# Kernel optimization log

Measured on AMD Instinct MI355X. Metric: run time of the kernel, lower is better.

Reference implementation:

```python
import jax, jax.numpy as jnp
import numpy as np
from jax import lax

B, N, C_IN = 8, 4096, 64
NPOINT, K = 1024, 32
MLP = [128, 128, 256]
EPS = 1e-5


def setup_inputs() -> dict:
    key = jax.random.key(0)
    ks = jax.random.split(key, 2 + len(MLP))
    inp = {
        "xyz": jax.random.normal(ks[0], (B, N, 3), jnp.float32),
        "points": jax.random.normal(ks[1], (B, N, C_IN), jnp.float32),
    }
    last = 3 + C_IN
    for i, o in enumerate(MLP):
        inp[f"W{i}"] = jax.random.normal(ks[2 + i], (o, last), jnp.float32) / np.float32(np.sqrt(last))
        inp[f"b{i}"] = jnp.zeros((o,), jnp.float32)
        inp[f"gamma{i}"] = jnp.ones((o,), jnp.float32)
        inp[f"beta{i}"] = jnp.zeros((o,), jnp.float32)
        last = o
    return inp


def farthest_point_sample(xyz, S):
    # xyz: (B,N,3) -> idx (B,S). Deterministic start at index 0 (torch uses randint).
    Bn, Nn, _ = xyz.shape
    barange = jnp.arange(Bn)

    def step(carry, _):
        distance, farthest = carry
        centroid = xyz[barange, farthest][:, None, :]            # (B,1,3)
        d = jnp.sum((xyz - centroid) ** 2, axis=-1)              # (B,N)
        distance = jnp.minimum(distance, d)
        return (distance, jnp.argmax(distance, axis=-1)), farthest

    init = (jnp.full((Bn, Nn), 1e10, xyz.dtype), jnp.zeros((Bn,), jnp.int32))
    _, cent = lax.scan(step, init, None, length=S)
    return jnp.transpose(cent)                                    # (B,S)


def _sa_forward(xyz, points, params):
    S = min(NPOINT, N)
    Kk = min(K, N)
    fps_idx = farthest_point_sample(xyz, S)                       # (B,S)
    bidx = jnp.arange(xyz.shape[0])[:, None]
    new_xyz = xyz[bidx, fps_idx]                                  # (B,S,3)
    # squared distances (B,S,N)
    dists = (jnp.sum(new_xyz ** 2, -1, keepdims=True)
             - 2.0 * jnp.einsum('bsc,bnc->bsn', new_xyz, xyz)
             + jnp.sum(xyz ** 2, -1)[:, None, :])
    _, nn_idx = lax.top_k(-dists, Kk)                             # (B,S,K)
    bidx3 = jnp.arange(xyz.shape[0])[:, None, None]
    grouped_xyz = xyz[bidx3, nn_idx]                              # (B,S,K,3)
    grouped_xyz_norm = grouped_xyz - new_xyz[:, :, None, :]
    grouped_pts = points[bidx3, nn_idx]                           # (B,S,K,C)
    feat = jnp.concatenate([grouped_xyz_norm, grouped_pts], -1)   # (B,S,K,3+C)
    for (W, b, g, be) in params:
        feat = jnp.einsum('bskc,oc->bsko', feat, W) + b           # 1x1 conv
        mean = jnp.mean(feat, axis=(0, 1, 2))
        var = jnp.var(feat, axis=(0, 1, 2))                        # biased, training-mode BN
        feat = (feat - mean) * lax.rsqrt(var + EPS) * g + be
        feat = jax.nn.relu(feat)
    out = jnp.max(feat, axis=2)                                   # max over K -> (B,S,O)
    return new_xyz, jnp.transpose(out, (0, 2, 1))                 # (B,O,S) like torch


def reference(xyz, points, W0, b0, gamma0, beta0, W1, b1, gamma1, beta1, W2, b2, gamma2, beta2):
    params = [(W0, b0, gamma0, beta0), (W1, b1, gamma1, beta1), (W2, b2, gamma2, beta2)]
    return _sa_forward(xyz, points, params)
```

## Files before the change

kernel.cpp:

```cpp
#include <hip/hip_runtime.h>
#include <cstdint>
#include <cstddef>

typedef _Float16 half8 __attribute__((ext_vector_type(8)));
typedef float f32x4 __attribute__((ext_vector_type(4)));
typedef float f32x2 __attribute__((ext_vector_type(2)));
typedef unsigned short ushort_t;

#define BB 8
#define NN 4096
#define CIN 64
#define SS 1024
#define KK 32
#define O1 128
#define O2 128
#define O3 256
#define C0 67
#define P0 104
#define P1 136
#define MTOT (BB*SS*KK)
#define NBLK 4096

__device__ __forceinline__ ushort_t f2h(float v) {
  union { _Float16 h; ushort_t u; } cv;
  cv.h = (_Float16)v;
  return cv.u;
}
__device__ __forceinline__ half8 ldv(const ushort_t* p) {
  return *(const half8*)p;
}
__device__ __forceinline__ f32x4 MF(half8 a, half8 b, f32x4 c) {
  return __builtin_amdgcn_mfma_f32_16x16x32_f16(a, b, c, 0, 0, 0);
}

template<bool MAXM>
__device__ __forceinline__ void wave_red_dpp(float& d, int& i) {
#define RED_TAKE(d2, i2) \
  { bool take = MAXM ? ((d2) > d || ((d2) == d && (i2) < i)) \
                     : ((d2) < d || ((d2) == d && (i2) < i)); \
    if (take) { d = (d2); i = (i2); } }
#define RED_DPP(CTRL) \
  { float d2_ = __int_as_float(__builtin_amdgcn_update_dpp(0, __float_as_int(d), CTRL, 0xf, 0xf, true)); \
    int   i2_ = __builtin_amdgcn_update_dpp(0, i, CTRL, 0xf, 0xf, true); \
    RED_TAKE(d2_, i2_) }
  RED_DPP(0x128)
  RED_DPP(0x124)
  RED_DPP(0x122)
  RED_DPP(0x121)
  RED_DPP(0x142)
  RED_DPP(0x143)
#undef RED_DPP
#undef RED_TAKE
}

__global__ __launch_bounds__(256, 1) void fps_kernel(const float* __restrict__ xyz,
                                                     float* __restrict__ newxyz) {
  int b = blockIdx.x, t = threadIdx.x;
  __shared__ float sxyz[NN*3];
  __shared__ float snew[SS*3];
  __shared__ __align__(16) float wpair[2][4][2];
  {
    const float4* src = (const float4*)(xyz + (size_t)b * (NN*3));
    float4* dst = (float4*)sxyz;
    for (int i = t; i < NN*3/4; i += 256) dst[i] = src[i];
  }
  __syncthreads();
  f32x2 px2[8], py2[8], pz2[8], d2[8];
#pragma unroll
  for (int j = 0; j < 8; ++j) {
    int n0 = t + 512*j, n1 = n0 + 256;
    f32x2 vx = {sxyz[n0*3+0], sxyz[n1*3+0]};
    f32x2 vy = {sxyz[n0*3+1], sxyz[n1*3+1]};
    f32x2 vz = {sxyz[n0*3+2], sxyz[n1*3+2]};
    px2[j] = vx; py2[j] = vy; pz2[j] = vz;
    f32x2 ini = {1e10f, 1e10f};
    d2[j] = ini;
  }
  float cx = sxyz[0], cy = sxyz[1], cz = sxyz[2];
  for (int s = 0; s < SS; ++s) {
    if (t == 0) {
      snew[s*3+0] = cx; snew[s*3+1] = cy; snew[s*3+2] = cz;
    }
    float bd0 = -1.f, bd1 = -1.f, bd2 = -1.f, bd3 = -1.f;
    int   bi0 = 0, bi1 = 0, bi2 = 0, bi3 = 0;
    {
#pragma clang fp contract(off)
      f32x2 c2x = {cx, cx}, c2y = {cy, cy}, c2z = {cz, cz};
#pragma unroll
      for (int j = 0; j < 8; ++j) {
        f32x2 dx = px2[j] - c2x;
        f32x2 dy = py2[j] - c2y;
        f32x2 dz = pz2[j] - c2z;
        f32x2 dd = (dx*dx + dy*dy) + dz*dz;
        float nd0 = fminf(d2[j][0], dd[0]);
        float nd1 = fminf(d2[j][1], dd[1]);
        d2[j][0] = nd0; d2[j][1] = nd1;
        int i0 = t + 512*j, i1 = i0 + 256;
        if ((j & 1) == 0) {
          if (nd0 > bd0) { bd0 = nd0; bi0 = i0; }
          if (nd1 > bd1) { bd1 = nd1; bi1 = i1; }
        } else {
          if (nd0 > bd2) { bd2 = nd0; bi2 = i0; }
          if (nd1 > bd3) { bd3 = nd1; bi3 = i1; }
        }
      }
    }
    float bd = bd0; int bi = bi0;
    if (bd1 > bd || (bd1 == bd && bi1 < bi)) { bd = bd1; bi = bi1; }
    if (bd2 > bd || (bd2 == bd && bi2 < bi)) { bd = bd2; bi = bi2; }
    if (bd3 > bd || (bd3 == bd && bi3 < bi)) { bd = bd3; bi = bi3; }

    wave_red_dpp<true>(bd, bi);

    int p = s & 1;
    if ((t & 63) == 63) {
      wpair[p][t>>6][0] = bd;
      ((int*)&wpair[p][t>>6][0])[1] = bi;
    }
    __syncthreads();
    float4 q0 = *(const float4*)&wpair[p][0][0];
    float4 q1 = *(const float4*)&wpair[p][2][0];
    float fd = q0.x; int fi = __float_as_int(q0.y);
#define CMB(dv, iv) { float od = (dv); int oi = __float_as_int(iv); \
      if (od > fd || (od == fd && oi < fi)) { fd = od; fi = oi; } }
    CMB(q0.z, q0.w) CMB(q1.x, q1.y) CMB(q1.z, q1.w)
#undef CMB
    cx = sxyz[fi*3+0]; cy = sxyz[fi*3+1]; cz = sxyz[fi*3+2];
  }
  __syncthreads();
  {
    float4* dst = (float4*)(newxyz + (size_t)b * (SS*3));
    const float4* src = (const float4*)snew;
    for (int i = t; i < SS*3/4; i += 256) dst[i] = src[i];
  }
}

__global__ __launch_bounds__(256) void knn_kernel(const float* __restrict__ xyz,
                                                  const float* __restrict__ newxyz,
                                                  int* __restrict__ nn) {
  int blk = blockIdx.x;
  int b = blk >> 10;
  int t = threadIdx.x;
  __shared__ __align__(16) float lpair[2][4][2];
  __shared__ int sidx[KK];
  float qx = newxyz[(size_t)blk*3+0];
  float qy = newxyz[(size_t)blk*3+1];
  float qz = newxyz[(size_t)blk*3+2];
  float cs = __fadd_rn(__fadd_rn(__fmul_rn(qx,qx), __fmul_rn(qy,qy)), __fmul_rn(qz,qz));
  const float* base = xyz + (size_t)b * (NN*3);
  float d[16];
#pragma unroll
  for (int j = 0; j < 16; ++j) {
    int n = t + 256*j;
    float px = base[n*3+0], py = base[n*3+1], pz = base[n*3+2];
    float xs  = __fadd_rn(__fadd_rn(__fmul_rn(px,px), __fmul_rn(py,py)), __fmul_rn(pz,pz));
    float dot = __fadd_rn(__fadd_rn(__fmul_rn(qx,px), __fmul_rn(qy,py)), __fmul_rn(qz,pz));
    d[j] = __fadd_rn(__fadd_rn(cs, -__fmul_rn(2.f, dot)), xs);
  }
  float lmin = 3.0e38f; int lidx = 0x7fffffff;
#pragma unroll
  for (int j = 0; j < 16; ++j) {
    if (d[j] < lmin) { lmin = d[j]; lidx = t + 256*j; }
  }
  for (int it = 0; it < KK; ++it) {
    float bd = lmin; int bi = lidx;
    wave_red_dpp<false>(bd, bi);
    int p = it & 1;
    if ((t & 63) == 63) {
      lpair[p][t>>6][0] = bd;
      ((int*)&lpair[p][t>>6][0])[1] = bi;
    }
    __syncthreads();
    float4 q0 = *(const float4*)&lpair[p][0][0];
    float4 q1 = *(const float4*)&lpair[p][2][0];
    float fd = q0.x; int fi = __float_as_int(q0.y);
#define CMB(dv, iv) { float od = (dv); int oi = __float_as_int(iv); \
      if (od < fd || (od == fd && oi < fi)) { fd = od; fi = oi; } }
    CMB(q0.z, q0.w) CMB(q1.x, q1.y) CMB(q1.z, q1.w)
#undef CMB
    if (t == 0) sidx[it] = fi;
    if ((fi & 255) == t) {
      int jj = fi >> 8;
#pragma unroll
      for (int j = 0; j < 16; ++j) if (j == jj) d[j] = 3.0e38f;
      lmin = 3.0e38f; lidx = 0x7fffffff;
#pragma unroll
      for (int j = 0; j < 16; ++j) {
        if (d[j] < lmin) { lmin = d[j]; lidx = t + 256*j; }
      }
    }
  }
  __syncthreads();
  if (t < KK) nn[(size_t)blk*KK + t] = sidx[t];
}

__global__ void prep_kernel(const float* __restrict__ W0, const float* __restrict__ W1,
                            const float* __restrict__ W2,
                            ushort_t* __restrict__ wb1, ushort_t* __restrict__ wb2,
                            ushort_t* __restrict__ wb3) {
  int i = blockIdx.x*256 + threadIdx.x;
  int stride = gridDim.x*256;
  const int n1 = O1*96, n2 = O2*128, n3 = O3*128;
  for (; i < n1+n2+n3; i += stride) {
    if (i < n1) {
      int o = i / 96, k = i - o*96;
      wb1[i] = (k < C0) ? f2h(W0[o*C0 + k]) : (ushort_t)0;
    } else if (i < n1+n2) {
      int j = i - n1;
      wb2[j] = f2h(W1[j]);
    } else {
      int j = i - n1 - n2;
      wb3[j] = f2h(W2[j]);
    }
  }
}

template<int NT>
__device__ __forceinline__ void stats_and_store(
    const f32x4* acc, const float* __restrict__ bias,
    float (*sred)[256][2],
    int w, int lr, int lg, int t, int blk,
    float* __restrict__ psum, float* __restrict__ psq)
{
#pragma unroll
  for (int n = 0; n < NT; ++n) {
    int c = n*16 + lr;
    float bi = bias[c];
    float x0 = acc[n][0]+bi, x1 = acc[n][1]+bi, x2 = acc[n][2]+bi, x3 = acc[n][3]+bi;
    float s4 = (x0+x1)+(x2+x3);
    float q4 = (x0*x0+x1*x1)+(x2*x2+x3*x3);
    s4 += __shfl_xor(s4, 16); s4 += __shfl_xor(s4, 32);
    q4 += __shfl_xor(q4, 16); q4 += __shfl_xor(q4, 32);
    if (lg == 0) { sred[w][c][0] = s4; sred[w][c][1] = q4; }
  }
  __syncthreads();
  if (t < NT*16) {
    float ps = (sred[0][t][0]+sred[1][t][0])+(sred[2][t][0]+sred[3][t][0]);
    float pq = (sred[0][t][1]+sred[1][t][1])+(sred[2][t][1]+sred[3][t][1]);
    psum[(size_t)t*NBLK + blk] = ps;
    psq [(size_t)t*NBLK + blk] = pq;
  }
}

__device__ __forceinline__ void stage_feat0(
    const float* __restrict__ xyz, const float* __restrict__ points,
    const float* __restrict__ newxyz, const int* __restrict__ nn,
    ushort_t* sF, int t, int b, int pr)
{
  int r = t >> 2, q = t & 3;
  int gi = r >> 5, j = r & 31;
  int bs = (b << 10) + (pr*2 + gi);
  int idx = nn[(size_t)bs*KK + j];
  const float* prow = points + ((size_t)(b*NN + idx))*CIN;
  const float* pxyz = xyz    + ((size_t)(b*NN + idx))*3;
  const float* ctr  = newxyz + (size_t)bs*3;
  ushort_t* dst = &sF[r*P0];
  if (q < 3) dst[q] = f2h(pxyz[q] - ctr[q]);
#pragma unroll
  for (int ii = 0; ii < 4; ++ii) {
    float4 v = *(const float4*)&prow[q*4 + ii*16];
    int c = 3 + q*4 + ii*16;
    dst[c+0] = f2h(v.x); dst[c+1] = f2h(v.y); dst[c+2] = f2h(v.z); dst[c+3] = f2h(v.w);
  }
  for (int c = C0 + q; c < P0; c += 4) dst[c] = 0;
}

__global__ __launch_bounds__(256) void conv1_kernel(
    const float* __restrict__ xyz, const float* __restrict__ points,
    const float* __restrict__ newxyz, const int* __restrict__ nn,
    const ushort_t* __restrict__ wb1, const float* __restrict__ bias1,
    ushort_t* __restrict__ z, float* __restrict__ psum, float* __restrict__ psq)
{
  __shared__ __align__(16) ushort_t sF[64*P0];
  __shared__ __align__(16) ushort_t s1[64*P1];
  __shared__ float sred[4][O1][2];
  int t = threadIdx.x, blk = blockIdx.x;
  int b = blk >> 9, pr = blk & 511;

  stage_feat0(xyz, points, newxyz, nn, sF, t, b, pr);
  __syncthreads();

  int w = t >> 6, l = t & 63;
  int lr = l & 15, lg = l >> 4;
  int ko = lg * 8;
  int arow = w*16 + lr;

  half8 a0 = ldv(&sF[arow*P0 +  0 + ko]);
  half8 a1 = ldv(&sF[arow*P0 + 32 + ko]);
  half8 a2 = ldv(&sF[arow*P0 + 64 + ko]);
  f32x4 acc1[8];
#pragma unroll
  for (int n = 0; n < 8; ++n) {
    const ushort_t* wrow = wb1 + (size_t)(n*16 + lr)*96 + ko;
    f32x4 c = {0.f,0.f,0.f,0.f};
    c = MF(a0, ldv(wrow +  0), c);
    c = MF(a1, ldv(wrow + 32), c);
    c = MF(a2, ldv(wrow + 64), c);
    acc1[n] = c;
  }

#pragma unroll
  for (int n = 0; n < 8; ++n) {
    int c = n*16 + lr;
#pragma unroll
    for (int rr = 0; rr < 4; ++rr)
      s1[(w*16 + lg*4 + rr)*P1 + c] = f2h(acc1[n][rr]);
    float bi = bias1[c];
    float x0 = acc1[n][0]+bi, x1 = acc1[n][1]+bi, x2 = acc1[n][2]+bi, x3 = acc1[n][3]+bi;
    float s4 = (x0+x1)+(x2+x3);
    float q4 = (x0*x0+x1*x1)+(x2*x2+x3*x3);
    s4 += __shfl_xor(s4, 16); s4 += __shfl_xor(s4, 32);
    q4 += __shfl_xor(q4, 16); q4 += __shfl_xor(q4, 32);
    if (lg == 0) { sred[w][c][0] = s4; sred[w][c][1] = q4; }
  }
  __syncthreads();
  {
    size_t chunk = (size_t)blk * (64*128);
#pragma unroll
    for (int i = 0; i < 4; ++i) {
      int off = t*8 + i*2048;
      *(half8*)&z[chunk + off] = ldv(&s1[(off>>7)*P1 + (off&127)]);
    }
  }
  if (t < O1) {
    float ps = (sred[0][t][0]+sred[1][t][0])+(sred[2][t][0]+sred[3][t][0]);
    float pq = (sred[0][t][1]+sred[1][t][1])+(sred[2][t][1]+sred[3][t][1]);
    psum[(size_t)t*NBLK + blk] = ps;
    psq [(size_t)t*NBLK + blk] = pq;
  }
}

__global__ __launch_bounds__(256) void conv2_kernel(
    ushort_t* __restrict__ z, const ushort_t* __restrict__ wb2,
    const float* __restrict__ bias2,
    const float* __restrict__ aa1, const float* __restrict__ bb1,
    float* __restrict__ psum, float* __restrict__ psq)
{
  __shared__ __align__(16) ushort_t s1[64*P1];
  __shared__ float sred[4][O2][2];
  int t = threadIdx.x, blk = blockIdx.x;
  size_t chunk = (size_t)blk * (64*128);

  int c0 = (t*8) & 127;
  float av[8], bv[8];
  {
    float4 alo = *(const float4*)&aa1[c0], ahi = *(const float4*)&aa1[c0+4];
    float4 blo = *(const float4*)&bb1[c0], bhi = *(const float4*)&bb1[c0+4];
    av[0]=alo.x; av[1]=alo.y; av[2]=alo.z; av[3]=alo.w;
    av[4]=ahi.x; av[5]=ahi.y; av[6]=ahi.z; av[7]=ahi.w;
    bv[0]=blo.x; bv[1]=blo.y; bv[2]=blo.z; bv[3]=blo.w;
    bv[4]=bhi.x; bv[5]=bhi.y; bv[6]=bhi.z; bv[7]=bhi.w;
  }
#pragma unroll
  for (int i = 0; i < 4; ++i) {
    int off = t*8 + i*2048;
    half8 v = ldv(&z[chunk + off]);
    half8 y;
#pragma unroll
    for (int jj = 0; jj < 8; ++jj)
      y[jj] = (_Float16)fmaxf(av[jj]*(float)v[jj] + bv[jj], 0.f);
    *(half8*)&s1[(off>>7)*P1 + c0] = y;
  }
  __syncthreads();

  int w = t >> 6, l = t & 63;
  int lr = l & 15, lg = l >> 4;
  int ko = lg * 8;
  int arow = w*16 + lr;

  half8 f0 = ldv(&s1[arow*P1 +  0 + ko]);
  half8 f1 = ldv(&s1[arow*P1 + 32 + ko]);
  half8 f2 = ldv(&s1[arow*P1 + 64 + ko]);
  half8 f3 = ldv(&s1[arow*P1 + 96 + ko]);
  f32x4 acc2[8];
#pragma unroll
  for (int n = 0; n < 8; ++n) {
    const ushort_t* wrow = wb2 + (size_t)(n*16 + lr)*128 + ko;
    f32x4 c = {0.f,0.f,0.f,0.f};
    c = MF(f0, ldv(wrow +  0), c);
    c = MF(f1, ldv(wrow + 32), c);
    c = MF(f2, ldv(wrow + 64), c);
    c = MF(f3, ldv(wrow + 96), c);
    acc2[n] = c;
  }
  __syncthreads();

#pragma unroll
  for (int n = 0; n < 8; ++n) {
    int c = n*16 + lr;
#pragma unroll
    for (int rr = 0; rr < 4; ++rr)
      s1[(w*16 + lg*4 + rr)*P1 + c] = f2h(acc2[n][rr]);
    float bi = bias2[c];
    float x0 = acc2[n][0]+bi, x1 = acc2[n][1]+bi, x2 = acc2[n][2]+bi, x3 = acc2[n][3]+bi;
    float s4 = (x0+x1)+(x2+x3);
    float q4 = (x0*x0+x1*x1)+(x2*x2+x3*x3);
    s4 += __shfl_xor(s4, 16); s4 += __shfl_xor(s4, 32);
    q4 += __shfl_xor(q4, 16); q4 += __shfl_xor(q4, 32);
    if (lg == 0) { sred[w][c][0] = s4; sred[w][c][1] = q4; }
  }
  __syncthreads();
#pragma unroll
  for (int i = 0; i < 4; ++i) {
    int off = t*8 + i*2048;
    *(half8*)&z[chunk + off] = ldv(&s1[(off>>7)*P1 + (off&127)]);
  }
  if (t < O2) {
    float ps = (sred[0][t][0]+sred[1][t][0])+(sred[2][t][0]+sred[3][t][0]);
    float pq = (sred[0][t][1]+sred[1][t][1])+(sred[2][t][1]+sred[3][t][1]);
    psum[(size_t)t*NBLK + blk] = ps;
    psq [(size_t)t*NBLK + blk] = pq;
  }
}

__global__ __launch_bounds__(256) void conv3_kernel(
    const ushort_t* __restrict__ z, const ushort_t* __restrict__ wb3,
    const float* __restrict__ bias3,
    const float* __restrict__ aa2, const float* __restrict__ bb2,
    float* __restrict__ psum, float* __restrict__ psq,
    float* __restrict__ maxb, float* __restrict__ minb)
{
  __shared__ __align__(16) ushort_t s2[64*P1];
  __shared__ float sred[4][O3][2];
  __shared__ float smm[4][O3][2];
  int t = threadIdx.x, blk = blockIdx.x;
  int b = blk >> 9, pr = blk & 511;
  size_t chunk = (size_t)blk * (64*128);

  int c0 = (t*8) & 127;
  float av[8], bv[8];
  {
    float4 alo = *(const float4*)&aa2[c0], ahi = *(const float4*)&aa2[c0+4];
    float4 blo = *(const float4*)&bb2[c0], bhi = *(const float4*)&bb2[c0+4];
    av[0]=alo.x; av[1]=alo.y; av[2]=alo.z; av[3]=alo.w;
    av[4]=ahi.x; av[5]=ahi.y; av[6]=ahi.z; av[7]=ahi.w;
    bv[0]=blo.x; bv[1]=blo.y; bv[2]=blo.z; bv[3]=blo.w;
    bv[4]=bhi.x; bv[5]=bhi.y; bv[6]=bhi.z; bv[7]=bhi.w;
  }
#pragma unroll
  for (int i = 0; i < 4; ++i) {
    int off = t*8 + i*2048;
    half8 v = ldv(&z[chunk + off]);
    half8 y;
#pragma unroll
    for (int jj = 0; jj < 8; ++jj)
      y[jj] = (_Float16)fmaxf(av[jj]*(float)v[jj] + bv[jj], 0.f);
    *(half8*)&s2[(off>>7)*P1 + c0] = y;
  }
  __syncthreads();

  int w = t >> 6, l = t & 63;
  int lr = l & 15, lg = l >> 4;
  int ko = lg * 8;
  int arow = w*16 + lr;

  half8 g0 = ldv(&s2[arow*P1 +  0 + ko]);
  half8 g1 = ldv(&s2[arow*P1 + 32 + ko]);
  half8 g2 = ldv(&s2[arow*P1 + 64 + ko]);
  half8 g3 = ldv(&s2[arow*P1 + 96 + ko]);
  f32x4 acc3[16];
#pragma unroll
  for (int n = 0; n < 16; ++n) {
    const ushort_t* wrow = wb3 + (size_t)(n*16 + lr)*128 + ko;
    f32x4 c = {0.f,0.f,0.f,0.f};
    c = MF(g0, ldv(wrow +  0), c);
    c = MF(g1, ldv(wrow + 32), c);
    c = MF(g2, ldv(wrow + 64), c);
    c = MF(g3, ldv(wrow + 96), c);
    acc3[n] = c;
  }

#pragma unroll
  for (int n = 0; n < 16; ++n) {
    int c = n*16 + lr;
    float bi = bias3[c];
    float x0 = acc3[n][0]+bi, x1 = acc3[n][1]+bi, x2 = acc3[n][2]+bi, x3 = acc3[n][3]+bi;
    float s4 = (x0+x1)+(x2+x3);
    float q4 = (x0*x0+x1*x1)+(x2*x2+x3*x3);
    s4 += __shfl_xor(s4, 16); s4 += __shfl_xor(s4, 32);
    q4 += __shfl_xor(q4, 16); q4 += __shfl_xor(q4, 32);
    float mx = fmaxf(fmaxf(x0,x1), fmaxf(x2,x3));
    float mn = fminf(fminf(x0,x1), fminf(x2,x3));
    mx = fmaxf(mx, __shfl_xor(mx, 16)); mx = fmaxf(mx, __shfl_xor(mx, 32));
    mn = fminf(mn, __shfl_xor(mn, 16)); mn = fminf(mn, __shfl_xor(mn, 32));
    if (lg == 0) {
      sred[w][c][0] = s4; sred[w][c][1] = q4;
      smm[w][c][0] = mx; smm[w][c][1] = mn;
    }
  }
  __syncthreads();
  if (t < 256) {
    float ps = (sred[0][t][0]+sred[1][t][0])+(sred[2][t][0]+sred[3][t][0]);
    float pq = (sred[0][t][1]+sred[1][t][1])+(sred[2][t][1]+sred[3][t][1]);
    psum[(size_t)t*NBLK + blk] = ps;
    psq [(size_t)t*NBLK + blk] = pq;
#pragma unroll
    for (int gi2 = 0; gi2 < 2; ++gi2) {
      float mx = fmaxf(smm[gi2*2][t][0], smm[gi2*2+1][t][0]);
      float mn = fminf(smm[gi2*2][t][1], smm[gi2*2+1][t][1]);
      size_t o = ((size_t)(b*256 + t))*SS + (pr*2 + gi2);
      maxb[o] = mx; minb[o] = mn;
    }
  }
}

template<int DEPTH>
__global__ __launch_bounds__(256) void fused_kernel(
    const float* __restrict__ xyz, const float* __restrict__ points,
    const float* __restrict__ newxyz, const int* __restrict__ nn,
    const ushort_t* __restrict__ wb1, const ushort_t* __restrict__ wb2,
    const ushort_t* __restrict__ wb3,
    const float* __restrict__ bias1, const float* __restrict__ bias2,
    const float* __restrict__ bias3,
    const float* __restrict__ aa1, const float* __restrict__ bb1,
    const float* __restrict__ aa2, const float* __restrict__ bb2,
    float* __restrict__ psum, float* __restrict__ psq,
    float* __restrict__ maxb, float* __restrict__ minb)
{
  __shared__ __align__(16) ushort_t sF[64*P0];
  __shared__ __align__(16) ushort_t s1[(DEPTH>=2) ? 64*P1 : 8];
  __shared__ __align__(16) ushort_t s2[(DEPTH>=3) ? 64*P1 : 8];
  __shared__ float sred[4][256][2];
  __shared__ float smm[(DEPTH>=3)?4:1][256][2];

  int t = threadIdx.x, blk = blockIdx.x;
  int b = blk >> 9, pr = blk & 511;

  stage_feat0(xyz, points, newxyz, nn, sF, t, b, pr);
  __syncthreads();

  int w = t >> 6, l = t & 63;
  int lr = l & 15, lg = l >> 4;
  int ko = lg * 8;
  int arow = w*16 + lr;

  half8 a0 = ldv(&sF[arow*P0 +  0 + ko]);
  half8 a1 = ldv(&sF[arow*P0 + 32 + ko]);
  half8 a2 = ldv(&sF[arow*P0 + 64 + ko]);
  f32x4 acc1[8];
#pragma unroll
  for (int n = 0; n < 8; ++n) {
    const ushort_t* wrow = wb1 + (size_t)(n*16 + lr)*96 + ko;
    f32x4 c = {0.f,0.f,0.f,0.f};
    c = MF(a0, ldv(wrow +  0), c);
    c = MF(a1, ldv(wrow + 32), c);
    c = MF(a2, ldv(wrow + 64), c);
    acc1[n] = c;
  }

  if constexpr (DEPTH == 1) {
    stats_and_store<8>(acc1, bias1, sred, w, lr, lg, t, blk, psum, psq);
  } else {
#pragma unroll
    for (int n = 0; n < 8; ++n) {
      int c = n*16 + lr;
      float a = aa1[c], bo = bb1[c], bi = bias1[c];
#pragma unroll
      for (int rr = 0; rr < 4; ++rr) {
        float y = fmaxf(a*(acc1[n][rr] + bi) + bo, 0.f);
        s1[(w*16 + lg*4 + rr)*P1 + c] = f2h(y);
      }
    }
    __syncthreads();

    half8 f0 = ldv(&s1[arow*P1 +  0 + ko]);
    half8 f1 = ldv(&s1[arow*P1 + 32 + ko]);
    half8 f2 = ldv(&s1[arow*P1 + 64 + ko]);
    half8 f3 = ldv(&s1[arow*P1 + 96 + ko]);
    f32x4 acc2[8];
#pragma unroll
    for (int n = 0; n < 8; ++n) {
      const ushort_t* wrow = wb2 + (size_t)(n*16 + lr)*128 + ko;
      f32x4 c = {0.f,0.f,0.f,0.f};
      c = MF(f0, ldv(wrow +  0), c);
      c = MF(f1, ldv(wrow + 32), c);
      c = MF(f2, ldv(wrow + 64), c);
      c = MF(f3, ldv(wrow + 96), c);
      acc2[n] = c;
    }

    if constexpr (DEPTH == 2) {
      stats_and_store<8>(acc2, bias2, sred, w, lr, lg, t, blk, psum, psq);
    } else {
#pragma unroll
      for (int n = 0; n < 8; ++n) {
        int c = n*16 + lr;
        float a = aa2[c], bo = bb2[c], bi = bias2[c];
#pragma unroll
        for (int rr = 0; rr < 4; ++rr) {
          float y = fmaxf(a*(acc2[n][rr] + bi) + bo, 0.f);
          s2[(w*16 + lg*4 + rr)*P1 + c] = f2h(y);
        }
      }
      __syncthreads();

      half8 g0 = ldv(&s2[arow*P1 +  0 + ko]);
      half8 g1 = ldv(&s2[arow*P1 + 32 + ko]);
      half8 g2 = ldv(&s2[arow*P1 + 64 + ko]);
      half8 g3 = ldv(&s2[arow*P1 + 96 + ko]);
      f32x4 acc3[16];
#pragma unroll
      for (int n = 0; n < 16; ++n) {
        const ushort_t* wrow = wb3 + (size_t)(n*16 + lr)*128 + ko;
        f32x4 c = {0.f,0.f,0.f,0.f};
        c = MF(g0, ldv(wrow +  0), c);
        c = MF(g1, ldv(wrow + 32), c);
        c = MF(g2, ldv(wrow + 64), c);
        c = MF(g3, ldv(wrow + 96), c);
        acc3[n] = c;
      }

#pragma unroll
      for (int n = 0; n < 16; ++n) {
        int c = n*16 + lr;
        float bi = bias3[c];
        float x0 = acc3[n][0]+bi, x1 = acc3[n][1]+bi, x2 = acc3[n][2]+bi, x3 = acc3[n][3]+bi;
        float s4 = (x0+x1)+(x2+x3);
        float q4 = (x0*x0+x1*x1)+(x2*x2+x3*x3);
        s4 += __shfl_xor(s4, 16); s4 += __shfl_xor(s4, 32);
        q4 += __shfl_xor(q4, 16); q4 += __shfl_xor(q4, 32);
        float mx = fmaxf(fmaxf(x0,x1), fmaxf(x2,x3));
        float mn = fminf(fminf(x0,x1), fminf(x2,x3));
        mx = fmaxf(mx, __shfl_xor(mx, 16)); mx = fmaxf(mx, __shfl_xor(mx, 32));
        mn = fminf(mn, __shfl_xor(mn, 16)); mn = fminf(mn, __shfl_xor(mn, 32));
        if (lg == 0) {
          sred[w][c][0] = s4; sred[w][c][1] = q4;
          smm[w][c][0] = mx; smm[w][c][1] = mn;
        }
      }
      __syncthreads();
      if (t < 256) {
        float ps = (sred[0][t][0]+sred[1][t][0])+(sred[2][t][0]+sred[3][t][0]);
        float pq = (sred[0][t][1]+sred[1][t][1])+(sred[2][t][1]+sred[3][t][1]);
        psum[(size_t)t*NBLK + blk] = ps;
        psq [(size_t)t*NBLK + blk] = pq;
#pragma unroll
        for (int gi2 = 0; gi2 < 2; ++gi2) {
          float mx = fmaxf(smm[gi2*2][t][0], smm[gi2*2+1][t][0]);
          float mn = fminf(smm[gi2*2][t][1], smm[gi2*2+1][t][1]);
          size_t o = ((size_t)(b*256 + t))*SS + (pr*2 + gi2);
          maxb[o] = mx; minb[o] = mn;
        }
      }
    }
  }
}

__global__ __launch_bounds__(256) void bnstats_finalize_kernel(
    const float* __restrict__ psum, const float* __restrict__ psq,
    const float* __restrict__ gamma, const float* __restrict__ beta,
    const float* __restrict__ bias, int fold,
    float* __restrict__ aa, float* __restrict__ bb)
{
  int c = blockIdx.x, t = threadIdx.x;
  double s = 0.0, q = 0.0;
  for (int i = t; i < NBLK; i += 256) {
    s += (double)psum[(size_t)c*NBLK + i];
    q += (double)psq [(size_t)c*NBLK + i];
  }
#pragma unroll
  for (int m = 1; m <= 32; m <<= 1) { s += __shfl_xor(s, m); q += __shfl_xor(q, m); }
  __shared__ double sd[4][2];
  if ((t & 63) == 0) { sd[t>>6][0] = s; sd[t>>6][1] = q; }
  __syncthreads();
  if (t == 0) {
    double S = (sd[0][0]+sd[1][0])+(sd[2][0]+sd[3][0]);
    double Q = (sd[0][1]+sd[1][1])+(sd[2][1]+sd[3][1]);
    double mean = S / (double)MTOT;
    double var  = Q / (double)MTOT - mean*mean;
    double rs = 1.0 / sqrt(var + 1e-5);
    double a = (double)gamma[c] * rs;
    aa[c] = (float)a;
    double bbv = (double)beta[c] - mean * a;
    if (fold) bbv += a * (double)bias[c];
    bb[c] = (float)bbv;
  }
}

__global__ __launch_bounds__(256) void final_out_kernel(
    const float* __restrict__ aa, const float* __restrict__ bb,
    const float* __restrict__ maxb, const float* __restrict__ minb,
    float* __restrict__ out2)
{
  int blk = blockIdx.x;
  int c = blk & 255;
  float a = aa[c], bo = bb[c];
  const float* src = (a >= 0.f) ? maxb : minb;
  size_t base = (size_t)blk * SS;
  for (int s = threadIdx.x; s < SS; s += 256)
    out2[base + s] = fmaxf(fmaf(a, src[base + s], bo), 0.f);
}

extern "C" void kernel_launch(void* const* d_in, const int* in_sizes, int n_in,
                              void* d_out, int out_size, void* d_ws, size_t ws_size,
                              hipStream_t stream) {
  const float* xyz    = (const float*)d_in[0];
  const float* points = (const float*)d_in[1];
  const float* W0 = (const float*)d_in[2];
  const float* b0 = (const float*)d_in[3];
  const float* g0 = (const float*)d_in[4];
  const float* be0= (const float*)d_in[5];
  const float* W1 = (const float*)d_in[6];
  const float* b1 = (const float*)d_in[7];
  const float* g1 = (const float*)d_in[8];
  const float* be1= (const float*)d_in[9];
  const float* W2 = (const float*)d_in[10];
  const float* b2 = (const float*)d_in[11];
  const float* g2 = (const float*)d_in[12];
  const float* be2= (const float*)d_in[13];

  float* out = (float*)d_out;
  float* newxyz = out;
  float* out2   = out + BB*SS*3;

  char* ws = (char*)d_ws;
  int*      nn   = (int*)ws;
  ushort_t* wb1  = (ushort_t*)(ws + 0x100000);
  ushort_t* wb2  = (ushort_t*)(ws + 0x106000);
  ushort_t* wb3  = (ushort_t*)(ws + 0x10E000);
  float* aa1 = (float*)(ws + 0x11E000);
  float* bb1 = aa1 + 128;
  float* aa2 = bb1 + 128;
  float* bb2 = aa2 + 128;
  float* aa3 = bb2 + 128;
  float* bb3 = aa3 + 256;
  float* psum1 = (float*)(ws + 0x120000);
  float* psq1  = (float*)(ws + 0x320000);
  float* psum2 = (float*)(ws + 0x520000);
  float* psq2  = (float*)(ws + 0x720000);
  float* psum3 = (float*)(ws + 0x920000);
  float* psq3  = (float*)(ws + 0xD20000);
  float* maxb  = (float*)(ws + 0x1120000);
  float* minb  = (float*)(ws + 0x1920000);
  ushort_t* z  = (ushort_t*)(ws + 0x2120000);
  const size_t NEEDED = 0x6120000ull;

  prep_kernel<<<64, 256, 0, stream>>>(W0, W1, W2, wb1, wb2, wb3);
  fps_kernel<<<BB, 256, 0, stream>>>(xyz, newxyz);
  knn_kernel<<<BB*SS, 256, 0, stream>>>(xyz, newxyz, nn);

  if (ws_size >= NEEDED) {
    conv1_kernel<<<NBLK, 256, 0, stream>>>(xyz, points, newxyz, nn, wb1, b0,
                                           z, psum1, psq1);
    bnstats_finalize_kernel<<<O1, 256, 0, stream>>>(psum1, psq1, g0, be0, b0, 1, aa1, bb1);
    conv2_kernel<<<NBLK, 256, 0, stream>>>(z, wb2, b1, aa1, bb1, psum2, psq2);
    bnstats_finalize_kernel<<<O2, 256, 0, stream>>>(psum2, psq2, g1, be1, b1, 1, aa2, bb2);
    conv3_kernel<<<NBLK, 256, 0, stream>>>(z, wb3, b2, aa2, bb2, psum3, psq3, maxb, minb);
    bnstats_finalize_kernel<<<O3, 256, 0, stream>>>(psum3, psq3, g2, be2, b2, 0, aa3, bb3);
  } else {
    fused_kernel<1><<<NBLK, 256, 0, stream>>>(xyz, points, newxyz, nn, wb1, wb2, wb3,
        b0, b1, b2, aa1, bb1, aa2, bb2, psum1, psq1, maxb, minb);
    bnstats_finalize_kernel<<<O1, 256, 0, stream>>>(psum1, psq1, g0, be0, b0, 0, aa1, bb1);
    fused_kernel<2><<<NBLK, 256, 0, stream>>>(xyz, points, newxyz, nn, wb1, wb2, wb3,
        b0, b1, b2, aa1, bb1, aa2, bb2, psum2, psq2, maxb, minb);
    bnstats_finalize_kernel<<<O2, 256, 0, stream>>>(psum2, psq2, g1, be1, b1, 0, aa2, bb2);
    fused_kernel<3><<<NBLK, 256, 0, stream>>>(xyz, points, newxyz, nn, wb1, wb2, wb3,
        b0, b1, b2, aa1, bb1, aa2, bb2, psum3, psq3, maxb, minb);
    bnstats_finalize_kernel<<<O3, 256, 0, stream>>>(psum3, psq3, g2, be2, b2, 0, aa3, bb3);
  }

  final_out_kernel<<<BB*O3, 256, 0, stream>>>(aa3, bb3, maxb, minb, out2);
}
```

Baseline: 1.551 ms.

## Assign one wavefront per KNN query with top-2 cache per lane

The KNN kernel now handles one query per 64-lane wavefront instead of one per 256-thread block, so each lane holds 64 distances. This removes the block-wide __syncthreads and shared-memory exchange from every selection iteration and uses a readlane broadcast instead. Each lane also keeps its two smallest distances, so the winning lane can often take its spare instead of rescanning. The cost is more registers per thread (64 distances), which may lower occupancy, and longer per-lane rescans when the spare runs out.

Result: slower. 1.862 ms (+20.1%).

```diff
diff --git a/kernel.cpp b/kernel.cpp
--- a/kernel.cpp
+++ b/kernel.cpp
@@ -138,60 +138,60 @@
 __global__ __launch_bounds__(256) void knn_kernel(const float* __restrict__ xyz,
                                                   const float* __restrict__ newxyz,
                                                   int* __restrict__ nn) {
-  int blk = blockIdx.x;
-  int b = blk >> 10;
   int t = threadIdx.x;
-  __shared__ __align__(16) float lpair[2][4][2];
-  __shared__ int sidx[KK];
-  float qx = newxyz[(size_t)blk*3+0];
-  float qy = newxyz[(size_t)blk*3+1];
-  float qz = newxyz[(size_t)blk*3+2];
+  int wv = t >> 6, lane = t & 63;
+  int qid = blockIdx.x * 4 + wv;
+  int b = qid >> 10;
+  __shared__ int sidx[4][KK];
+  float qx = newxyz[(size_t)qid*3+0];
+  float qy = newxyz[(size_t)qid*3+1];
+  float qz = newxyz[(size_t)qid*3+2];
   float cs = __fadd_rn(__fadd_rn(__fmul_rn(qx,qx), __fmul_rn(qy,qy)), __fmul_rn(qz,qz));
   const float* base = xyz + (size_t)b * (NN*3);
-  float d[16];
-#pragma unroll
-  for (int j = 0; j < 16; ++j) {
-    int n = t + 256*j;
+  float d[64];
+#pragma unroll
+  for (int j = 0; j < 64; ++j) {
+    int n = lane + 64*j;
     float px = base[n*3+0], py = base[n*3+1], pz = base[n*3+2];
     float xs  = __fadd_rn(__fadd_rn(__fmul_rn(px,px), __fmul_rn(py,py)), __fmul_rn(pz,pz));
     float dot = __fadd_rn(__fadd_rn(__fmul_rn(qx,px), __fmul_rn(qy,py)), __fmul_rn(qz,pz));
     d[j] = __fadd_rn(__fadd_rn(cs, -__fmul_rn(2.f, dot)), xs);
   }
-  float lmin = 3.0e38f; int lidx = 0x7fffffff;
-#pragma unroll
-  for (int j = 0; j < 16; ++j) {
-    if (d[j] < lmin) { lmin = d[j]; lidx = t + 256*j; }
-  }
+  float m1d = 3.0e38f, m2d = 3.0e38f;
+  int   m1i = 0x7fffffff, m2i = 0x7fffffff;
+#pragma unroll
+  for (int j = 0; j < 64; ++j) {
+    float dj = d[j]; int i = lane + 64*j;
+    if (dj < m1d)      { m2d = m1d; m2i = m1i; m1d = dj; m1i = i; }
+    else if (dj < m2d) { m2d = dj; m2i = i; }
+  }
+  bool spare = true;
   for (int it = 0; it < KK; ++it) {
-    float bd = lmin; int bi = lidx;
+    float bd = m1d; int bi = m1i;
     wave_red_dpp<false>(bd, bi);
-    int p = it & 1;
-    if ((t & 63) == 63) {
-      lpair[p][t>>6][0] = bd;
-      ((int*)&lpair[p][t>>6][0])[1] = bi;
-    }
-    __syncthreads();
-    float4 q0 = *(const float4*)&lpair[p][0][0];
-    float4 q1 = *(const float4*)&lpair[p][2][0];
-    float fd = q0.x; int fi = __float_as_int(q0.y);
-#define CMB(dv, iv) { float od = (dv); int oi = __float_as_int(iv); \
-      if (od < fd || (od == fd && oi < fi)) { fd = od; fi = oi; } }
-    CMB(q0.z, q0.w) CMB(q1.x, q1.y) CMB(q1.z, q1.w)
-#undef CMB
-    if (t == 0) sidx[it] = fi;
-    if ((fi & 255) == t) {
-      int jj = fi >> 8;
-#pragma unroll
-      for (int j = 0; j < 16; ++j) if (j == jj) d[j] = 3.0e38f;
-      lmin = 3.0e38f; lidx = 0x7fffffff;
-#pragma unroll
-      for (int j = 0; j < 16; ++j) {
-        if (d[j] < lmin) { lmin = d[j]; lidx = t + 256*j; }
+    int   fi = __builtin_amdgcn_readlane(bi, 63);
+    float fd = __int_as_float(__builtin_amdgcn_readlane(__float_as_int(bd), 63));
+    if (lane == 0) sidx[wv][it] = fi;
+    if ((fi & 63) == lane) {
+      if (spare) {
+        m1d = m2d; m1i = m2i; spare = false;
+      } else {
+        m1d = 3.0e38f; m1i = 0x7fffffff; m2d = 3.0e38f; m2i = 0x7fffffff;
+#pragma unroll
+        for (int j = 0; j < 64; ++j) {
+          float dj = d[j]; int i = lane + 64*j;
+          bool valid = (dj > fd) || (dj == fd && i > fi);
+          if (valid) {
+            if (dj < m1d)      { m2d = m1d; m2i = m1i; m1d = dj; m1i = i; }
+            else if (dj < m2d) { m2d = dj; m2i = i; }
+          }
+        }
+        spare = true;
       }
     }
   }
   __syncthreads();
-  if (t < KK) nn[(size_t)blk*KK + t] = sidx[t];
+  if (t < 4*KK) nn[(size_t)blockIdx.x * (4*KK) + t] = sidx[t>>5][t&31];
 }
 
 __global__ void prep_kernel(const float* __restrict__ W0, const float* __restrict__ W1,
@@ -737,7 +737,7 @@
 
   prep_kernel<<<64, 256, 0, stream>>>(W0, W1, W2, wb1, wb2, wb3);
   fps_kernel<<<BB, 256, 0, stream>>>(xyz, newxyz);
-  knn_kernel<<<BB*SS, 256, 0, stream>>>(xyz, newxyz, nn);
+  knn_kernel<<<BB*SS/4, 256, 0, stream>>>(xyz, newxyz, nn);
 
   if (ws_size >= NEEDED) {
     conv1_kernel<<<NBLK, 256, 0, stream>>>(xyz, points, newxyz, nn, wb1, b0,
```
